# Kernel tuning notes

Measured on AMD Instinct MI355X. Metric: run time of the kernel, lower is better.

The kernel has to match this reference:

```python
import jax, jax.numpy as jnp
import numpy as np

B, H, C, N, K_TERMS = 256, 512, 64, 100, 8


def eval_cubic_spline(coeffs, tobs, t):
    # coeffs: [B, N-1, 4, C]; tobs: [N] sorted knots; t: scalar
    idx = jnp.clip(jnp.searchsorted(tobs, t, side='right') - 1, 0, tobs.shape[0] - 2)
    dt = t - tobs[idx]
    c = coeffs[:, idx]  # [B, 4, C]
    # Horner evaluation: c0 + c1*dt + c2*dt^2 + c3*dt^3
    return c[:, 0] + dt * (c[:, 1] + dt * (c[:, 2] + dt * c[:, 3]))


def setup_inputs() -> dict:
    key = jax.random.key(0)
    k_h, k_c, k_dc, k_wx, k_wh, k_wo = jax.random.split(key, 6)
    xav = lambda k, shape: jax.random.uniform(
        k, shape, minval=-1.0, maxval=1.0, dtype=jnp.float32
    ) * np.float32(np.sqrt(6.0 / (shape[0] + shape[1])))
    return {
        't': jnp.float32(0.5),
        'h': jax.random.normal(k_h, (B, H), dtype=jnp.float32),
        'coeffs': jax.random.normal(k_c, (B, N - 1, 4, C), dtype=jnp.float32),
        'dcoeffs': jax.random.normal(k_dc, (B, N - 1, 4, C), dtype=jnp.float32),
        'tobs': jnp.linspace(0.0, 1.0, N, dtype=jnp.float32),
        'wx': xav(k_wx, (H, C)),
        'wh': xav(k_wh, (H, H)),
        'wout': xav(k_wo, (H, H)),
        'b0': jnp.zeros((H,), dtype=jnp.float32),
        'b1': jnp.zeros((H,), dtype=jnp.float32),
    }


def reference(t, h, coeffs, dcoeffs, tobs, wx, wh, wout, b0, b1):
    x = eval_cubic_spline(coeffs, tobs, t)      # [B, C]
    xdot = eval_cubic_spline(dcoeffs, tobs, t)  # [B, C]
    l1 = x @ wx.T + h @ wh.T + b0               # [B, H]
    relu = jnp.maximum(l1, 0.0)
    th = jnp.tanh(relu @ wout.T + b1)           # [B, H]
    dtanh = 1.0 - th * th
    drelu = jax.nn.sigmoid(l1)                  # surrogate_relu branch
    # Jacobian assembly via broadcasted outer product: [B, H, H]
    d_outer = dtanh[:, :, None] * wout[None, :, :] * drelu[:, None, :]
    Jx = d_outer @ wx                           # [B, H, C]
    Jh = d_outer @ wh                           # [B, H, H]
    curr = jnp.einsum('bhc,bc->bh', Jx, xdot)   # jx matvec, [B, H]
    h_dot = curr
    for _ in range(K_TERMS):                    # Neumann-series recurrence
        curr = jnp.einsum('bij,bj->bi', Jh, curr)
        h_dot = h_dot + curr
    return h_dot
```

## Files before the change

kernel.cpp:

```cpp
#include <hip/hip_runtime.h>

#define BB 256
#define HH 512
#define CC 64
#define NN 100
#define KT 8

typedef short s16x8 __attribute__((ext_vector_type(8)));
typedef float f32x4 __attribute__((ext_vector_type(4)));

#define MFMA16(a, b, c) __builtin_amdgcn_mfma_f32_16x16x32_bf16((a), (b), (c), 0, 0, 0)

static __device__ __forceinline__ unsigned short f2bf(float f) {
    union { float f; unsigned int u; } v; v.f = f;
    unsigned int r = v.u + 0x7FFFu + ((v.u >> 16) & 1u);
    return (unsigned short)(r >> 16);
}


__global__ void k_pack(const float* __restrict__ wh, const float* __restrict__ wout,
                       const float* __restrict__ wx, const float* __restrict__ h,
                       const float* __restrict__ coeffs, const float* __restrict__ dcoeffs,
                       const float* __restrict__ tobs, const float* __restrict__ tg,
                       unsigned short* __restrict__ whp, unsigned short* __restrict__ wop,
                       unsigned short* __restrict__ wxp, unsigned short* __restrict__ hb,
                       unsigned short* __restrict__ xb, unsigned short* __restrict__ xdb) {
    int gid = blockIdx.x * 256 + threadIdx.x;
    if (gid < 524288) {
        const float* src = (gid < 262144) ? wh : wout;
        unsigned short* dst = (gid < 262144) ? whp : wop;
        int p = gid & 262143;
        int e = p & 7, lane = (p >> 3) & 63, g = (p >> 9) & 15, cg = (p >> 13) & 1, w = p >> 14;
        int row = w * 32 + cg * 16 + (lane & 15);
        int k = g * 32 + (lane >> 4) * 8 + e;
        dst[p] = f2bf(src[row * HH + k]);
    } else if (gid < 557056) {
        int p = gid - 524288;
        int e = p & 7, lane = (p >> 3) & 63, g = (p >> 9) & 1, cg = (p >> 10) & 1, w = p >> 11;
        int row = w * 32 + cg * 16 + (lane & 15);
        int k = g * 32 + (lane >> 4) * 8 + e;
        wxp[p] = f2bf(wx[row * CC + k]);
    } else if (gid < 688128) {
        int p = gid - 557056;
        hb[p] = f2bf(h[p]);
    } else if (gid < 704512) {
        int p = gid - 688128;
        int b = p >> 6, c = p & 63;
        float t = tg[0];
        int cntv = 0;
        for (int n = 0; n < NN; n++) cntv += (tobs[n] <= t) ? 1 : 0;
        int idx = cntv - 1;
        idx = idx < 0 ? 0 : (idx > NN - 2 ? NN - 2 : idx);
        float dt = t - tobs[idx];
        const float* cb = coeffs + ((size_t)(b * (NN - 1) + idx) * 4) * CC + c;
        float xv = cb[0] + dt * (cb[CC] + dt * (cb[2 * CC] + dt * cb[3 * CC]));
        const float* db = dcoeffs + ((size_t)(b * (NN - 1) + idx) * 4) * CC + c;
        float xd = db[0] + dt * (db[CC] + dt * (db[2 * CC] + dt * db[3 * CC]));
        xb[p] = f2bf(xv);
        xdb[p] = f2bf(xd);
    }
}

__global__ void k_l1(const unsigned short* __restrict__ whp, const unsigned short* __restrict__ wxp,
                     const unsigned short* __restrict__ hb, const unsigned short* __restrict__ xb,
                     const unsigned short* __restrict__ xdb, const float* __restrict__ b0g,
                     unsigned short* __restrict__ relu_b, float* __restrict__ drelu_f,
                     unsigned short* __restrict__ s0_b) {
    __shared__ unsigned short sh[32][520];
    __shared__ unsigned short sx[32][72];
    __shared__ unsigned short sxd[32][72];
    int tid = threadIdx.x;
    int b0 = blockIdx.x * 32;
    int it = blockIdx.y;
    for (int idx = tid; idx < 32 * 64; idx += 256) {
        int r = idx >> 6, c8 = idx & 63;
        *(int4*)&sh[r][c8 * 8] = *(const int4*)&hb[(b0 + r) * HH + c8 * 8];
    }
    for (int idx = tid; idx < 32 * 8; idx += 256) {
        int r = idx >> 3, c8 = idx & 7;
        *(int4*)&sx[r][c8 * 8] = *(const int4*)&xb[(b0 + r) * CC + c8 * 8];
        *(int4*)&sxd[r][c8 * 8] = *(const int4*)&xdb[(b0 + r) * CC + c8 * 8];
    }
    __syncthreads();
    int wv = tid >> 6, lane = tid & 63, col = lane & 15, kq = lane >> 4;
    int isub = it * 64 + wv * 16;
    int wpk = isub >> 5, cg = (isub >> 4) & 1;
    f32x4 acc0 = {0.f, 0.f, 0.f, 0.f}, acc1 = {0.f, 0.f, 0.f, 0.f};
    f32x4 vac0 = {0.f, 0.f, 0.f, 0.f}, vac1 = {0.f, 0.f, 0.f, 0.f};
    const s16x8* whfrag = (const s16x8*)whp + (size_t)((wpk * 2 + cg) * 16) * 64 + lane;
#pragma unroll
    for (int g = 0; g < 16; g++) {
        s16x8 bf = whfrag[g * 64];
        s16x8 a0 = *(const s16x8*)&sh[col][g * 32 + kq * 8];
        s16x8 a1 = *(const s16x8*)&sh[16 + col][g * 32 + kq * 8];
        acc0 = MFMA16(a0, bf, acc0);
        acc1 = MFMA16(a1, bf, acc1);
    }
    const s16x8* wxfrag = (const s16x8*)wxp + (size_t)((wpk * 2 + cg) * 2) * 64 + lane;
#pragma unroll
    for (int g = 0; g < 2; g++) {
        s16x8 bf = wxfrag[g * 64];
        s16x8 a0 = *(const s16x8*)&sx[col][g * 32 + kq * 8];
        s16x8 a1 = *(const s16x8*)&sx[16 + col][g * 32 + kq * 8];
        acc0 = MFMA16(a0, bf, acc0);
        acc1 = MFMA16(a1, bf, acc1);
        s16x8 d0 = *(const s16x8*)&sxd[col][g * 32 + kq * 8];
        s16x8 d1 = *(const s16x8*)&sxd[16 + col][g * 32 + kq * 8];
        vac0 = MFMA16(d0, bf, vac0);
        vac1 = MFMA16(d1, bf, vac1);
    }
    int ic = isub + col;
    float bias = b0g[ic];
#pragma unroll
    for (int r = 0; r < 4; r++) {
        int bb = b0 + kq * 4 + r;
        float l1a = acc0[r] + bias;
        float dra = 1.f / (1.f + expf(-l1a));
        relu_b[bb * HH + ic] = f2bf(fmaxf(l1a, 0.f));
        drelu_f[bb * HH + ic] = dra;
        s0_b[bb * HH + ic] = f2bf(dra * vac0[r]);
        float l1b = acc1[r] + bias;
        float drb = 1.f / (1.f + expf(-l1b));
        relu_b[(bb + 16) * HH + ic] = f2bf(fmaxf(l1b, 0.f));
        drelu_f[(bb + 16) * HH + ic] = drb;
        s0_b[(bb + 16) * HH + ic] = f2bf(drb * vac1[r]);
    }
}

__global__ void k_th(const unsigned short* __restrict__ wop, const unsigned short* __restrict__ relu_b,
                     const unsigned short* __restrict__ s0_b, const float* __restrict__ b1g,
                     float* __restrict__ dtanh_f, unsigned short* __restrict__ curr_b,
                     float* __restrict__ curr0_f) {
    __shared__ unsigned short sr[32][520];
    __shared__ unsigned short ss0[32][520];
    int tid = threadIdx.x;
    int b0 = blockIdx.x * 32;
    int it = blockIdx.y;
    for (int idx = tid; idx < 32 * 64; idx += 256) {
        int r = idx >> 6, c8 = idx & 63;
        *(int4*)&sr[r][c8 * 8] = *(const int4*)&relu_b[(b0 + r) * HH + c8 * 8];
        *(int4*)&ss0[r][c8 * 8] = *(const int4*)&s0_b[(b0 + r) * HH + c8 * 8];
    }
    __syncthreads();
    int wv = tid >> 6, lane = tid & 63, col = lane & 15, kq = lane >> 4;
    int isub = it * 64 + wv * 16;
    int wpk = isub >> 5, cg = (isub >> 4) & 1;
    f32x4 acc0 = {0.f, 0.f, 0.f, 0.f}, acc1 = {0.f, 0.f, 0.f, 0.f};
    f32x4 cac0 = {0.f, 0.f, 0.f, 0.f}, cac1 = {0.f, 0.f, 0.f, 0.f};
    const s16x8* wofrag = (const s16x8*)wop + (size_t)((wpk * 2 + cg) * 16) * 64 + lane;
#pragma unroll
    for (int g = 0; g < 16; g++) {
        s16x8 bf = wofrag[g * 64];
        s16x8 a0 = *(const s16x8*)&sr[col][g * 32 + kq * 8];
        s16x8 a1 = *(const s16x8*)&sr[16 + col][g * 32 + kq * 8];
        acc0 = MFMA16(a0, bf, acc0);
        acc1 = MFMA16(a1, bf, acc1);
        s16x8 p0 = *(const s16x8*)&ss0[col][g * 32 + kq * 8];
        s16x8 p1 = *(const s16x8*)&ss0[16 + col][g * 32 + kq * 8];
        cac0 = MFMA16(p0, bf, cac0);
        cac1 = MFMA16(p1, bf, cac1);
    }
    int ic = isub + col;
    float bias = b1g[ic];
    int fc = (ic >> 5) * 512 + (ic & 7) + (((ic >> 3) & 3) << 7);
#pragma unroll
    for (int r = 0; r < 4; r++) {
        int bb = b0 + kq * 4 + r;
        int row8 = (kq * 4 + r) * 8;
        float th_a = tanhf(acc0[r] + bias);
        float dta = 1.f - th_a * th_a;
        float c0a = dta * cac0[r];
        dtanh_f[bb * HH + ic] = dta;
        curr_b[(bb >> 4) * 8192 + fc + row8] = f2bf(c0a);
        curr0_f[bb * HH + ic] = c0a;
        float th_b = tanhf(acc1[r] + bias);
        float dtb = 1.f - th_b * th_b;
        float c0b = dtb * cac1[r];
        dtanh_f[(bb + 16) * HH + ic] = dtb;
        curr_b[((bb + 16) >> 4) * 8192 + fc + row8] = f2bf(c0b);
        curr0_f[(bb + 16) * HH + ic] = c0b;
    }
}

__global__ __launch_bounds__(1024) void k_loop5(
    const unsigned short* __restrict__ whp, const unsigned short* __restrict__ wop,
    const unsigned short* __restrict__ curr_b, const float* __restrict__ curr0_f,
    const float* __restrict__ drelu_f, const float* __restrict__ dtanh_f,
    float* __restrict__ outp) {
    __shared__ __align__(16) unsigned short sa[2][8192];
    const int tid = threadIdx.x;
    const int w = tid >> 6, lane = tid & 63;
    const int col2 = lane & 15, kq = lane >> 4;
    const int bt = blockIdx.x;

    {
        const int4* src = (const int4*)(curr_b + (size_t)bt * 8192);
        ((int4*)&sa[0][0])[tid] = src[tid];
    }

    float dr[2][4], dt[2][4], hd[2][4];
#pragma unroll
    for (int t = 0; t < 2; t++) {
        const int c = (w * 2 + t) * 16 + col2;
#pragma unroll
        for (int r = 0; r < 4; r++) {
            const int row = bt * 16 + kq * 4 + r;
            dr[t][r] = drelu_f[row * HH + c];
            dt[t][r] = dtanh_f[row * HH + c];
            hd[t][r] = curr0_f[row * HH + c];
        }
    }

    int fb[2];
#pragma unroll
    for (int t = 0; t < 2; t++)
        fb[t] = w * 512 + (col2 & 7) + (((t * 2 + (col2 >> 3)) & 3) << 7) + kq * 32;

    const s16x8* wlh = (const s16x8*)whp + (size_t)w * 2048 + lane;
    const s16x8* wlo = (const s16x8*)wop + (size_t)w * 2048 + lane;
    const unsigned short* A0 = &sa[0][lane * 8];
    const unsigned short* A1 = &sa[1][lane * 8];

    __syncthreads();

    for (int p = 0; p < 16; p++) {
        const s16x8* wl = (p & 1) ? wlo : wlh;
        const unsigned short* Ar = (p & 1) ? A1 : A0;
        f32x4 acc[2] = {{0.f, 0.f, 0.f, 0.f}, {0.f, 0.f, 0.f, 0.f}};
        s16x8 bfr[2][2];
#pragma unroll
        for (int t = 0; t < 2; t++) bfr[0][t] = wl[t * 1024];
#pragma unroll
        for (int g = 0; g < 16; g++) {
            if (g < 15) {
#pragma unroll
                for (int t = 0; t < 2; t++) bfr[(g + 1) & 1][t] = wl[t * 1024 + (g + 1) * 64];
            }
            const s16x8 a = *(const s16x8*)(Ar + (size_t)g * 512);
#pragma unroll
            for (int t = 0; t < 2; t++) acc[t] = MFMA16(a, bfr[g & 1][t], acc[t]);
        }
        unsigned short* Aw = &sa[(p + 1) & 1][0];
        if (p & 1) {
            if (p < 15) {
#pragma unroll
                for (int t = 0; t < 2; t++)
#pragma unroll
                    for (int r = 0; r < 4; r++) {
                        float v = dt[t][r] * acc[t][r];
                        hd[t][r] += v;
                        Aw[fb[t] + r * 8] = f2bf(v);
                    }
            } else {
#pragma unroll
                for (int t = 0; t < 2; t++)
#pragma unroll
                    for (int r = 0; r < 4; r++) hd[t][r] += dt[t][r] * acc[t][r];
            }
        } else {
#pragma unroll
            for (int t = 0; t < 2; t++)
#pragma unroll
                for (int r = 0; r < 4; r++)
                    Aw[fb[t] + r * 8] = f2bf(dr[t][r] * acc[t][r]);
        }
        if (p < 15) __syncthreads();
    }

#pragma unroll
    for (int t = 0; t < 2; t++) {
        const int c = (w * 2 + t) * 16 + col2;
#pragma unroll
        for (int r = 0; r < 4; r++)
            outp[(size_t)(bt * 16 + kq * 4 + r) * HH + c] = hd[t][r];
    }
}

extern "C" void kernel_launch(void* const* d_in, const int* in_sizes, int n_in,
                              void* d_out, int out_size, void* d_ws, size_t ws_size,
                              hipStream_t stream) {
    const float* tg = (const float*)d_in[0];
    const float* h = (const float*)d_in[1];
    const float* coeffs = (const float*)d_in[2];
    const float* dcoeffs = (const float*)d_in[3];
    const float* tobs = (const float*)d_in[4];
    const float* wx = (const float*)d_in[5];
    const float* wh = (const float*)d_in[6];
    const float* wout = (const float*)d_in[7];
    const float* b0g = (const float*)d_in[8];
    const float* b1g = (const float*)d_in[9];
    float* outp = (float*)d_out;

    char* ws = (char*)d_ws;
    unsigned short* whp    = (unsigned short*)(ws + 0);
    unsigned short* wop    = (unsigned short*)(ws + 524288);
    unsigned short* wxp    = (unsigned short*)(ws + 1048576);
    unsigned short* hb     = (unsigned short*)(ws + 1114112);
    unsigned short* xb     = (unsigned short*)(ws + 1376256);
    unsigned short* xdb    = (unsigned short*)(ws + 1409024);
    unsigned short* relu_b = (unsigned short*)(ws + 1441792);
    unsigned short* s0_b   = (unsigned short*)(ws + 1703936);
    float* drelu_f         = (float*)(ws + 1966080);
    float* dtanh_f         = (float*)(ws + 2490368);
    unsigned short* curr_b = (unsigned short*)(ws + 3014656);
    float* curr0_f         = (float*)(ws + 3276800);

    k_pack<<<2752, 256, 0, stream>>>(wh, wout, wx, h, coeffs, dcoeffs, tobs, tg,
                                     whp, wop, wxp, hb, xb, xdb);
    k_l1<<<dim3(8, 8), 256, 0, stream>>>(whp, wxp, hb, xb, xdb, b0g, relu_b, drelu_f, s0_b);
    k_th<<<dim3(8, 8), 256, 0, stream>>>(wop, relu_b, s0_b, b1g, dtanh_f, curr_b, curr0_f);
    k_loop5<<<16, 1024, 0, stream>>>(whp, wop, curr_b, curr0_f, drelu_f, dtanh_f, outp);
}
```

Before: 181.8 us.

## Split Neumann loop across block pairs with global flag exchange of half-vectors

The recurrence kernel moves from 16 blocks of 1024 threads to 32 blocks of 512 threads. Each pair of blocks shares one 16-row batch tile and splits the 512 output columns between them. After each step, each block writes its half of the next input vector to a global exchange buffer and signals a per-step flag. Its partner spins on that flag before loading the half, which halves the weight bytes streamed per block and doubles the number of CUs in use. In exchange, every step adds inter-block synchronisation and a global round trip. Correctness depends on all 32 blocks being resident at once, and the exchange buffer reuses the relu/s0 workspace region.

```diff
diff --git a/kernel.cpp b/kernel.cpp
--- a/kernel.cpp
+++ b/kernel.cpp
@@ -130,10 +130,14 @@
 __global__ void k_th(const unsigned short* __restrict__ wop, const unsigned short* __restrict__ relu_b,
                      const unsigned short* __restrict__ s0_b, const float* __restrict__ b1g,
                      float* __restrict__ dtanh_f, unsigned short* __restrict__ curr_b,
-                     float* __restrict__ curr0_f) {
+                     float* __restrict__ curr0_f, unsigned int* __restrict__ flg) {
     __shared__ unsigned short sr[32][520];
     __shared__ unsigned short ss0[32][520];
     int tid = threadIdx.x;
+    if (blockIdx.x == 0 && blockIdx.y == 0) {
+        flg[tid] = 0u;
+        flg[tid + 256] = 0u;
+    }
     int b0 = blockIdx.x * 32;
     int it = blockIdx.y;
     for (int idx = tid; idx < 32 * 64; idx += 256) {
@@ -182,48 +186,71 @@
     }
 }
 
-__global__ __launch_bounds__(1024) void k_loop5(
+__global__ __launch_bounds__(512) void k_loop6(
     const unsigned short* __restrict__ whp, const unsigned short* __restrict__ wop,
     const unsigned short* __restrict__ curr_b, const float* __restrict__ curr0_f,
     const float* __restrict__ drelu_f, const float* __restrict__ dtanh_f,
+    unsigned short* __restrict__ xch, unsigned int* flg,
     float* __restrict__ outp) {
     __shared__ __align__(16) unsigned short sa[2][8192];
     const int tid = threadIdx.x;
     const int w = tid >> 6, lane = tid & 63;
     const int col2 = lane & 15, kq = lane >> 4;
-    const int bt = blockIdx.x;
+    const int c = blockIdx.x & 15;
+    const int s = blockIdx.x >> 4;
 
     {
-        const int4* src = (const int4*)(curr_b + (size_t)bt * 8192);
-        ((int4*)&sa[0][0])[tid] = src[tid];
+        const int4* src = (const int4*)(curr_b + (size_t)c * 8192);
+        int4* dst = (int4*)&sa[0][0];
+        dst[tid] = src[tid];
+        dst[tid + 512] = src[tid + 512];
     }
 
     float dr[2][4], dt[2][4], hd[2][4];
 #pragma unroll
     for (int t = 0; t < 2; t++) {
-        const int c = (w * 2 + t) * 16 + col2;
+        const int cc = s * 256 + (w * 2 + t) * 16 + col2;
 #pragma unroll
         for (int r = 0; r < 4; r++) {
-            const int row = bt * 16 + kq * 4 + r;
-            dr[t][r] = drelu_f[row * HH + c];
-            dt[t][r] = dtanh_f[row * HH + c];
-            hd[t][r] = curr0_f[row * HH + c];
-        }
-    }
-
-    int fb[2];
+            const int row = c * 16 + kq * 4 + r;
+            dr[t][r] = drelu_f[row * HH + cc];
+            dt[t][r] = dtanh_f[row * HH + cc];
+            hd[t][r] = curr0_f[row * HH + cc];
+        }
+    }
+
+    int fbl[2];
 #pragma unroll
     for (int t = 0; t < 2; t++)
-        fb[t] = w * 512 + (col2 & 7) + (((t * 2 + (col2 >> 3)) & 3) << 7) + kq * 32;
-
-    const s16x8* wlh = (const s16x8*)whp + (size_t)w * 2048 + lane;
-    const s16x8* wlo = (const s16x8*)wop + (size_t)w * 2048 + lane;
+        fbl[t] = w * 512 + (col2 & 7) + (((t * 2 + (col2 >> 3)) & 3) << 7) + kq * 32;
+    const int myhalf = s * 4096;
+    const int phalf = (1 - s) * 4096;
+
+    const s16x8* wlh = (const s16x8*)whp + (size_t)(s * 16 + w * 2) * 1024 + lane;
+    const s16x8* wlo = (const s16x8*)wop + (size_t)(s * 16 + w * 2) * 1024 + lane;
     const unsigned short* A0 = &sa[0][lane * 8];
     const unsigned short* A1 = &sa[1][lane * 8];
+    unsigned int* fme = flg + (s * 16 + c) * 16;
+    unsigned int* fpr = flg + ((1 - s) * 16 + c) * 16;
 
     __syncthreads();
 
     for (int p = 0; p < 16; p++) {
+        if (p) {
+            if (tid == 0) {
+                while (__hip_atomic_load(fpr, __ATOMIC_RELAXED, __HIP_MEMORY_SCOPE_AGENT)
+                       < (unsigned)p) { __builtin_amdgcn_s_sleep(1); }
+            }
+            __syncthreads();
+            const unsigned long long* gsrc = (const unsigned long long*)
+                (xch + ((size_t)(c * 2 + ((p - 1) & 1)) * 2 + (1 - s)) * 4096);
+            unsigned long long v0 = __hip_atomic_load(&gsrc[tid], __ATOMIC_RELAXED, __HIP_MEMORY_SCOPE_AGENT);
+            unsigned long long v1 = __hip_atomic_load(&gsrc[tid + 512], __ATOMIC_RELAXED, __HIP_MEMORY_SCOPE_AGENT);
+            unsigned long long* ld = (unsigned long long*)&sa[p & 1][phalf];
+            ld[tid] = v0;
+            ld[tid + 512] = v1;
+            __syncthreads();
+        }
         const s16x8* wl = (p & 1) ? wlo : wlh;
         const unsigned short* Ar = (p & 1) ? A1 : A0;
         f32x4 acc[2] = {{0.f, 0.f, 0.f, 0.f}, {0.f, 0.f, 0.f, 0.f}};
@@ -249,7 +276,7 @@
                     for (int r = 0; r < 4; r++) {
                         float v = dt[t][r] * acc[t][r];
                         hd[t][r] += v;
-                        Aw[fb[t] + r * 8] = f2bf(v);
+                        Aw[myhalf + fbl[t] + r * 8] = f2bf(v);
                     }
             } else {
 #pragma unroll
@@ -262,17 +289,27 @@
             for (int t = 0; t < 2; t++)
 #pragma unroll
                 for (int r = 0; r < 4; r++)
-                    Aw[fb[t] + r * 8] = f2bf(dr[t][r] * acc[t][r]);
-        }
-        if (p < 15) __syncthreads();
+                    Aw[myhalf + fbl[t] + r * 8] = f2bf(dr[t][r] * acc[t][r]);
+        }
+        if (p < 15) {
+            __syncthreads();
+            unsigned long long* gdst = (unsigned long long*)
+                (xch + ((size_t)(c * 2 + (p & 1)) * 2 + s) * 4096);
+            const unsigned long long* lsrc = (const unsigned long long*)&sa[(p + 1) & 1][myhalf];
+            __hip_atomic_store(&gdst[tid], lsrc[tid], __ATOMIC_RELAXED, __HIP_MEMORY_SCOPE_AGENT);
+            __hip_atomic_store(&gdst[tid + 512], lsrc[tid + 512], __ATOMIC_RELAXED, __HIP_MEMORY_SCOPE_AGENT);
+            __syncthreads();
+            if (tid == 0)
+                __hip_atomic_store(fme, (unsigned)(p + 1), __ATOMIC_RELEASE, __HIP_MEMORY_SCOPE_AGENT);
+        }
     }
 
 #pragma unroll
     for (int t = 0; t < 2; t++) {
-        const int c = (w * 2 + t) * 16 + col2;
+        const int cc = s * 256 + (w * 2 + t) * 16 + col2;
 #pragma unroll
         for (int r = 0; r < 4; r++)
-            outp[(size_t)(bt * 16 + kq * 4 + r) * HH + c] = hd[t][r];
+            outp[(size_t)(c * 16 + kq * 4 + r) * HH + cc] = hd[t][r];
     }
 }
 
@@ -304,10 +341,12 @@
     float* dtanh_f         = (float*)(ws + 2490368);
     unsigned short* curr_b = (unsigned short*)(ws + 3014656);
     float* curr0_f         = (float*)(ws + 3276800);
+    unsigned short* xch    = (unsigned short*)(ws + 1441792);
+    unsigned int* flg      = (unsigned int*)(ws + 3801088);
 
     k_pack<<<2752, 256, 0, stream>>>(wh, wout, wx, h, coeffs, dcoeffs, tobs, tg,
                                      whp, wop, wxp, hb, xb, xdb);
     k_l1<<<dim3(8, 8), 256, 0, stream>>>(whp, wxp, hb, xb, xdb, b0g, relu_b, drelu_f, s0_b);
-    k_th<<<dim3(8, 8), 256, 0, stream>>>(wop, relu_b, s0_b, b1g, dtanh_f, curr_b, curr0_f);
-    k_loop5<<<16, 1024, 0, stream>>>(whp, wop, curr_b, curr0_f, drelu_f, dtanh_f, outp);
-}
+    k_th<<<dim3(8, 8), 256, 0, stream>>>(wop, relu_b, s0_b, b1g, dtanh_f, curr_b, curr0_f, flg);
+    k_loop6<<<32, 512, 0, stream>>>(whp, wop, curr_b, curr0_f, drelu_f, dtanh_f, xch, flg, outp);
+}
```

After: 171.1 us. 5.9% less time.
